# Optimization experiments

Hardware: AMD Instinct MI355X
Metric: run time of the kernel (lower is better)

The kernel has to match this reference:

```python
import jax, jax.numpy as jnp
import numpy as np

N = 100000   # nodes
E = 1600000  # edges
G = 256      # graphs in batch
C_IN = 128
D = 64
EPS = 1e-5
SLOPE = 0.01  # torch LeakyReLU default


def gcn_conv(h_x, src, dst, w_edge, W, b):
    """GCNConv: linear -> symmetric-normalized scatter aggregation (+ self loops) -> bias."""
    n = h_x.shape[0]
    h = h_x @ W                                   # [N, D]
    # add self loops with weight 1
    loop = jnp.arange(n, dtype=src.dtype)
    s = jnp.concatenate([src, loop])
    d = jnp.concatenate([dst, loop])
    w = jnp.concatenate([w_edge, jnp.ones((n,), h_x.dtype)])
    deg = jax.ops.segment_sum(w, d, num_segments=n)  # degree on target nodes
    dinv = jnp.where(deg > 0, jax.lax.rsqrt(jnp.maximum(deg, 1e-12)), 0.0)
    norm = dinv[s] * w * dinv[d]                  # [E+N]
    msg = h[s] * norm[:, None]                    # gather + scale
    out = jax.ops.segment_sum(msg, d, num_segments=n)
    return out + b


def batch_norm(h, gamma, beta):
    mean = jnp.mean(h, axis=0)
    var = jnp.mean((h - mean) ** 2, axis=0)       # biased var (training-mode BN)
    return (h - mean) * jax.lax.rsqrt(var + EPS) * gamma + beta


def setup_inputs() -> dict:
    key = jax.random.key(0)
    ks = jax.random.split(key, 16)
    inp = {
        "x": jax.random.normal(ks[0], (N, C_IN), jnp.float32),
        "edge_index": jax.random.randint(ks[1], (2, E), 0, N, jnp.int32),
        "batch": jnp.sort(jax.random.randint(ks[2], (N,), 0, G, jnp.int32)),
        "edge_attr": jax.random.uniform(ks[3], (E,), jnp.float32),
        "W0": jax.random.normal(ks[4], (C_IN, D), jnp.float32) * 0.05,
        "b0": jnp.zeros((D,), jnp.float32),
        "g0": jnp.ones((D,), jnp.float32),
        "be0": jnp.zeros((D,), jnp.float32),
        "W1": jax.random.normal(ks[5], (D, D), jnp.float32) * 0.05,
        "b1": jnp.zeros((D,), jnp.float32),
        "g1": jnp.ones((D,), jnp.float32),
        "be1": jnp.zeros((D,), jnp.float32),
        "W2": jax.random.normal(ks[6], (D, D), jnp.float32) * 0.05,
        "b2": jnp.zeros((D,), jnp.float32),
        "W3": jax.random.normal(ks[7], (D, D), jnp.float32) * 0.05,
        "b3": jnp.zeros((D,), jnp.float32),
        "Wfc": jax.random.normal(ks[8], (2 * D, 1), jnp.float32) * 0.05,
        "bfc": jnp.zeros((1,), jnp.float32),
    }
    return inp


def reference(x, edge_index, batch, edge_attr,
              W0, b0, g0, be0, W1, b1, g1, be1, W2, b2, W3, b3, Wfc, bfc):
    src, dst = edge_index[0], edge_index[1]
    lrelu = lambda h: jax.nn.leaky_relu(h, SLOPE)

    h = lrelu(batch_norm(gcn_conv(x, src, dst, edge_attr, W0, b0), g0, be0))
    h = lrelu(batch_norm(gcn_conv(h, src, dst, edge_attr, W1, b1), g1, be1))
    h = lrelu(gcn_conv(h, src, dst, edge_attr, W2, b2))  # dropout is identity in eval
    h = lrelu(gcn_conv(h, src, dst, edge_attr, W3, b3))

    mx = jax.ops.segment_max(h, batch, num_segments=G)
    sm = jax.ops.segment_sum(h, batch, num_segments=G)
    cnt = jax.ops.segment_sum(jnp.ones((N,), h.dtype), batch, num_segments=G)
    mean = sm / jnp.maximum(cnt, 1.0)[:, None]
    pooled = jnp.concatenate([mx, mean], axis=1)   # [G, 2D]
    return pooled @ Wfc + bfc                      # [G, 1]
```

## Files before the change

### kernel.cpp

```cpp
#include <hip/hip_runtime.h>
#include <math.h>

#define LRELU_SLOPE 0.01f
#define BN_EPS 1e-5f
#define WQ_SCALE 1048576.0f
#define WQ_INV   9.5367431640625e-7f

static inline int ceil_div(int a, int b) { return (a + b - 1) / b; }

__device__ __forceinline__ unsigned short f2bf(float f) {
  unsigned int u = __float_as_uint(f);
  u = u + 0x7FFFu + ((u >> 16) & 1u);
  return (unsigned short)(u >> 16);
}
#define BF2F(u) __uint_as_float(((unsigned int)(u)) << 16)

__launch_bounds__(1024)
__global__ void b1_hist(const int* __restrict__ ei, int* __restrict__ histT,
                        int E, int chunk, int nbuck) {
  __shared__ unsigned int hist[1024];
  const int t = threadIdx.x;
  const int blk = blockIdx.x;
  hist[t] = 0;
  __syncthreads();
  const int e0 = blk * chunk;
  const int e1 = min(e0 + chunk, E);
  for (int e = e0 + t; e < e1; e += 1024) {
    int d = ei[E + e];
    atomicAdd(&hist[d >> 7], 1u);
  }
  __syncthreads();
  if (t < nbuck) histT[(size_t)t * 256 + blk] = (int)hist[t];
}

__global__ void scan1i(const int* __restrict__ in, int* __restrict__ out,
                       int* __restrict__ bsum, int n) {
  __shared__ int lds[256];
  const int t = threadIdx.x;
  const int base = blockIdx.x * 1024 + t * 4;
  int v0 = 0, v1 = 0, v2 = 0, v3 = 0;
  if (base + 0 < n) v0 = in[base + 0];
  if (base + 1 < n) v1 = in[base + 1];
  if (base + 2 < n) v2 = in[base + 2];
  if (base + 3 < n) v3 = in[base + 3];
  int s = v0 + v1 + v2 + v3;
  lds[t] = s;
  __syncthreads();
#pragma unroll
  for (int off = 1; off < 256; off <<= 1) {
    int y = 0;
    if (t >= off) y = lds[t - off];
    __syncthreads();
    if (t >= off) lds[t] += y;
    __syncthreads();
  }
  int incl = lds[t];
  int excl = incl - s;
  if (base + 0 < n) out[base + 0] = excl;
  if (base + 1 < n) out[base + 1] = excl + v0;
  if (base + 2 < n) out[base + 2] = excl + v0 + v1;
  if (base + 3 < n) out[base + 3] = excl + v0 + v1 + v2;
  if (t == 255) bsum[blockIdx.x] = incl;
}

__global__ void scan2i(int* __restrict__ bsum, int nb) {
  __shared__ int lds[256];
  int t = threadIdx.x;
  int v = (t < nb) ? bsum[t] : 0;
  lds[t] = v;
  __syncthreads();
#pragma unroll
  for (int off = 1; off < 256; off <<= 1) {
    int y = 0;
    if (t >= off) y = lds[t - off];
    __syncthreads();
    if (t >= off) lds[t] += y;
    __syncthreads();
  }
  if (t < nb) bsum[t] = lds[t] - v;
}

__global__ void scan3i(int* __restrict__ data, const int* __restrict__ bscan, int n) {
  int i = blockIdx.x * blockDim.x + threadIdx.x;
  if (i < n) data[i] += bscan[i >> 10];
}

__launch_bounds__(1024)
__global__ void b3_scatter(const int* __restrict__ ei, const float* __restrict__ w,
                           const int* __restrict__ histS,
                           unsigned long long* __restrict__ bucketed,
                           int E, int chunk, int nbuck) {
  __shared__ unsigned int cursor[1024];
  const int t = threadIdx.x;
  const int blk = blockIdx.x;
  cursor[t] = (t < nbuck) ? (unsigned int)histS[(size_t)t * 256 + blk] : 0u;
  __syncthreads();
  const int e0 = blk * chunk;
  const int e1 = min(e0 + chunk, E);
  for (int e = e0 + t; e < e1; e += 1024) {
    int s = ei[e];
    int d = ei[E + e];
    unsigned int pos = atomicAdd(&cursor[d >> 7], 1u);
    unsigned long long p = ((unsigned long long)(unsigned int)(d & 127) << 57) |
                           ((unsigned long long)(unsigned int)s << 32) |
                           (unsigned long long)__float_as_uint(w[e]);
    bucketed[pos] = p;
  }
}

__launch_bounds__(256)
__global__ void c1_degree(const unsigned long long* __restrict__ bucketed,
                          const int* __restrict__ histS,
                          int* __restrict__ rowstart, float* __restrict__ dinv,
                          int N, int E, int nbuck) {
  __shared__ unsigned int cnt[128], wsum[128];
  __shared__ int sc[128];
  const int t = threadIdx.x;
  const int b = blockIdx.x;
  if (t < 128) { cnt[t] = 0; wsum[t] = 0; }
  __syncthreads();
  const int r0 = histS[(size_t)b * 256];
  const int r1 = (b + 1 < nbuck) ? histS[(size_t)(b + 1) * 256] : E;
  for (int r = r0 + t; r < r1; r += 256) {
    unsigned long long p = bucketed[r];
    int d7 = (int)(p >> 57);
    float wv = __uint_as_float((unsigned int)p);
    atomicAdd(&cnt[d7], 1u);
    atomicAdd(&wsum[d7], (unsigned int)__float2uint_rn(wv * WQ_SCALE));
  }
  __syncthreads();
  if (t < 128) sc[t] = (int)cnt[t];
  __syncthreads();
#pragma unroll
  for (int off = 1; off < 128; off <<= 1) {
    int y = 0;
    if (t < 128 && t >= off) y = sc[t - off];
    __syncthreads();
    if (t < 128 && t >= off) sc[t] += y;
    __syncthreads();
  }
  if (t < 128) {
    int node = (b << 7) + t;
    if (node < N) {
      rowstart[node] = r0 + sc[t] - (int)cnt[t];
      float deg = 1.0f + (float)wsum[t] * WQ_INV;
      dinv[node] = rsqrtf(deg);
    }
  }
  if (b == 0 && t == 0) rowstart[N] = E;
}

__launch_bounds__(256)
__global__ void c2_fill(const unsigned long long* __restrict__ bucketed,
                        const int* __restrict__ histS,
                        const int* __restrict__ rowstart, const float* __restrict__ dinv,
                        unsigned long long* __restrict__ colval,
                        int N, int E, int nbuck) {
  __shared__ unsigned int cursor[128];
  const int t = threadIdx.x;
  const int b = blockIdx.x;
  if (t < 128) {
    int node = (b << 7) + t;
    cursor[t] = (node < N) ? (unsigned int)rowstart[node] : 0u;
  }
  __syncthreads();
  const int r0 = histS[(size_t)b * 256];
  const int r1 = (b + 1 < nbuck) ? histS[(size_t)(b + 1) * 256] : E;
  for (int r = r0 + t; r < r1; r += 256) {
    unsigned long long p = bucketed[r];
    int d7 = (int)(p >> 57);
    int s = (int)((p >> 32) & 0x1FFFFFF);
    float wv = __uint_as_float((unsigned int)p);
    unsigned int pos = atomicAdd(&cursor[d7], 1u);
    float v = wv * dinv[s];
    colval[pos] = ((unsigned long long)(unsigned int)s << 32) |
                  (unsigned long long)__float_as_uint(v);
  }
}

template <int K, int BN>
__launch_bounds__(256, 4)
__global__ void k_gemm(const float* __restrict__ X, const float* __restrict__ W,
                       unsigned short* __restrict__ H16,
                       const float* __restrict__ s, const float* __restrict__ ss,
                       const float* __restrict__ g, const float* __restrict__ be,
                       int N) {
  __shared__ float Xl[64 * 68];
  __shared__ float Wl[64 * 64];
  __shared__ float scaleC[64], shiftC[64];
  const int t = threadIdx.x;
  const int tx = t & 15;
  const int ty = t >> 4;
  const int n0 = blockIdx.x * 64;

  if (BN) {
    if (t < 64) {
      float invN = 1.0f / (float)N;
      float mean = s[t] * invN;
      float var = ss[t] * invN - mean * mean;
      float sc = g[t] * rsqrtf(var + BN_EPS);
      scaleC[t] = sc;
      shiftC[t] = be[t] - mean * sc;
    }
  }

  float4 acc[4];
#pragma unroll
  for (int r = 0; r < 4; ++r) acc[r] = make_float4(0.f, 0.f, 0.f, 0.f);

  for (int kt = 0; kt < K; kt += 64) {
    __syncthreads();
#pragma unroll
    for (int l = 0; l < 4; ++l) {
      int idx = t + l * 256;
      int node = idx >> 4;
      int kq = idx & 15;
      int gn = n0 + node;
      float4 v = make_float4(0.f, 0.f, 0.f, 0.f);
      if (gn < N) v = *(const float4*)(X + (size_t)gn * K + kt + 4 * kq);
      int kb = 4 * kq;
      if (BN) {
        float a;
        a = v.x * scaleC[kb + 0] + shiftC[kb + 0]; v.x = (a > 0.f) ? a : LRELU_SLOPE * a;
        a = v.y * scaleC[kb + 1] + shiftC[kb + 1]; v.y = (a > 0.f) ? a : LRELU_SLOPE * a;
        a = v.z * scaleC[kb + 2] + shiftC[kb + 2]; v.z = (a > 0.f) ? a : LRELU_SLOPE * a;
        a = v.w * scaleC[kb + 3] + shiftC[kb + 3]; v.w = (a > 0.f) ? a : LRELU_SLOPE * a;
      }
      Xl[(kb + 0) * 68 + node] = v.x;
      Xl[(kb + 1) * 68 + node] = v.y;
      Xl[(kb + 2) * 68 + node] = v.z;
      Xl[(kb + 3) * 68 + node] = v.w;
    }
#pragma unroll
    for (int l = 0; l < 4; ++l) {
      int idx = t + l * 256;
      ((float4*)Wl)[idx] = *(const float4*)(W + (size_t)(kt + (idx >> 4)) * 64 + 4 * (idx & 15));
    }
    __syncthreads();
#pragma unroll 8
    for (int k = 0; k < 64; ++k) {
      float4 xv = *(const float4*)(Xl + k * 68 + 4 * ty);
      float4 wv = *(const float4*)(Wl + k * 64 + 4 * tx);
      acc[0].x += xv.x * wv.x; acc[0].y += xv.x * wv.y; acc[0].z += xv.x * wv.z; acc[0].w += xv.x * wv.w;
      acc[1].x += xv.y * wv.x; acc[1].y += xv.y * wv.y; acc[1].z += xv.y * wv.z; acc[1].w += xv.y * wv.w;
      acc[2].x += xv.z * wv.x; acc[2].y += xv.z * wv.y; acc[2].z += xv.z * wv.z; acc[2].w += xv.z * wv.w;
      acc[3].x += xv.w * wv.x; acc[3].y += xv.w * wv.y; acc[3].z += xv.w * wv.z; acc[3].w += xv.w * wv.w;
    }
  }
#pragma unroll
  for (int r = 0; r < 4; ++r) {
    int gn = n0 + 4 * ty + r;
    if (gn < N) {
      ushort4 o;
      o.x = f2bf(acc[r].x); o.y = f2bf(acc[r].y);
      o.z = f2bf(acc[r].z); o.w = f2bf(acc[r].w);
      *(ushort4*)(H16 + (size_t)gn * 64 + 4 * tx) = o;
    }
  }
}

__launch_bounds__(256)
__global__ void k_agg(const unsigned short* __restrict__ h16, float* __restrict__ hout,
                      const float* __restrict__ bias, const float* __restrict__ dinv,
                      const int* __restrict__ rowstart,
                      const unsigned long long* __restrict__ colval,
                      int N, int apply_lrelu) {
  const int t = threadIdx.x;
  const int grp = t >> 4;
  const int lane = t & 15;
  const int d = blockIdx.x * 16 + grp;
  if (d >= N) return;
  const int r0 = rowstart[d];
  const int r1 = rowstart[d + 1];
  float4 a0 = make_float4(0.f, 0.f, 0.f, 0.f);
  float4 a1 = make_float4(0.f, 0.f, 0.f, 0.f);
  float4 a2 = make_float4(0.f, 0.f, 0.f, 0.f);
  float4 a3 = make_float4(0.f, 0.f, 0.f, 0.f);
  int r = r0;
  for (; r + 8 <= r1; r += 8) {
    unsigned long long cv0 = colval[r + 0];
    unsigned long long cv1 = colval[r + 1];
    unsigned long long cv2 = colval[r + 2];
    unsigned long long cv3 = colval[r + 3];
    unsigned long long cv4 = colval[r + 4];
    unsigned long long cv5 = colval[r + 5];
    unsigned long long cv6 = colval[r + 6];
    unsigned long long cv7 = colval[r + 7];
    ushort4 h0 = *(const ushort4*)(h16 + ((size_t)(cv0 >> 32)) * 64 + lane * 4);
    ushort4 h1 = *(const ushort4*)(h16 + ((size_t)(cv1 >> 32)) * 64 + lane * 4);
    ushort4 h2 = *(const ushort4*)(h16 + ((size_t)(cv2 >> 32)) * 64 + lane * 4);
    ushort4 h3 = *(const ushort4*)(h16 + ((size_t)(cv3 >> 32)) * 64 + lane * 4);
    ushort4 h4 = *(const ushort4*)(h16 + ((size_t)(cv4 >> 32)) * 64 + lane * 4);
    ushort4 h5 = *(const ushort4*)(h16 + ((size_t)(cv5 >> 32)) * 64 + lane * 4);
    ushort4 h6 = *(const ushort4*)(h16 + ((size_t)(cv6 >> 32)) * 64 + lane * 4);
    ushort4 h7 = *(const ushort4*)(h16 + ((size_t)(cv7 >> 32)) * 64 + lane * 4);
    float v0 = __uint_as_float((unsigned int)cv0);
    float v1 = __uint_as_float((unsigned int)cv1);
    float v2 = __uint_as_float((unsigned int)cv2);
    float v3 = __uint_as_float((unsigned int)cv3);
    float v4 = __uint_as_float((unsigned int)cv4);
    float v5 = __uint_as_float((unsigned int)cv5);
    float v6 = __uint_as_float((unsigned int)cv6);
    float v7 = __uint_as_float((unsigned int)cv7);
    a0.x += v0 * BF2F(h0.x); a0.y += v0 * BF2F(h0.y); a0.z += v0 * BF2F(h0.z); a0.w += v0 * BF2F(h0.w);
    a1.x += v1 * BF2F(h1.x); a1.y += v1 * BF2F(h1.y); a1.z += v1 * BF2F(h1.z); a1.w += v1 * BF2F(h1.w);
    a2.x += v2 * BF2F(h2.x); a2.y += v2 * BF2F(h2.y); a2.z += v2 * BF2F(h2.z); a2.w += v2 * BF2F(h2.w);
    a3.x += v3 * BF2F(h3.x); a3.y += v3 * BF2F(h3.y); a3.z += v3 * BF2F(h3.z); a3.w += v3 * BF2F(h3.w);
    a0.x += v4 * BF2F(h4.x); a0.y += v4 * BF2F(h4.y); a0.z += v4 * BF2F(h4.z); a0.w += v4 * BF2F(h4.w);
    a1.x += v5 * BF2F(h5.x); a1.y += v5 * BF2F(h5.y); a1.z += v5 * BF2F(h5.z); a1.w += v5 * BF2F(h5.w);
    a2.x += v6 * BF2F(h6.x); a2.y += v6 * BF2F(h6.y); a2.z += v6 * BF2F(h6.z); a2.w += v6 * BF2F(h6.w);
    a3.x += v7 * BF2F(h7.x); a3.y += v7 * BF2F(h7.y); a3.z += v7 * BF2F(h7.z); a3.w += v7 * BF2F(h7.w);
  }
  for (; r + 4 <= r1; r += 4) {
    unsigned long long cv0 = colval[r + 0];
    unsigned long long cv1 = colval[r + 1];
    unsigned long long cv2 = colval[r + 2];
    unsigned long long cv3 = colval[r + 3];
    ushort4 h0 = *(const ushort4*)(h16 + ((size_t)(cv0 >> 32)) * 64 + lane * 4);
    ushort4 h1 = *(const ushort4*)(h16 + ((size_t)(cv1 >> 32)) * 64 + lane * 4);
    ushort4 h2 = *(const ushort4*)(h16 + ((size_t)(cv2 >> 32)) * 64 + lane * 4);
    ushort4 h3 = *(const ushort4*)(h16 + ((size_t)(cv3 >> 32)) * 64 + lane * 4);
    float v0 = __uint_as_float((unsigned int)cv0);
    float v1 = __uint_as_float((unsigned int)cv1);
    float v2 = __uint_as_float((unsigned int)cv2);
    float v3 = __uint_as_float((unsigned int)cv3);
    a0.x += v0 * BF2F(h0.x); a0.y += v0 * BF2F(h0.y); a0.z += v0 * BF2F(h0.z); a0.w += v0 * BF2F(h0.w);
    a1.x += v1 * BF2F(h1.x); a1.y += v1 * BF2F(h1.y); a1.z += v1 * BF2F(h1.z); a1.w += v1 * BF2F(h1.w);
    a2.x += v2 * BF2F(h2.x); a2.y += v2 * BF2F(h2.y); a2.z += v2 * BF2F(h2.z); a2.w += v2 * BF2F(h2.w);
    a3.x += v3 * BF2F(h3.x); a3.y += v3 * BF2F(h3.y); a3.z += v3 * BF2F(h3.z); a3.w += v3 * BF2F(h3.w);
  }
  for (; r < r1; ++r) {
    unsigned long long cv = colval[r];
    float v = __uint_as_float((unsigned int)cv);
    ushort4 hv = *(const ushort4*)(h16 + ((size_t)(cv >> 32)) * 64 + lane * 4);
    a0.x += v * BF2F(hv.x); a0.y += v * BF2F(hv.y); a0.z += v * BF2F(hv.z); a0.w += v * BF2F(hv.w);
  }
  float4 acc;
  acc.x = (a0.x + a1.x) + (a2.x + a3.x);
  acc.y = (a0.y + a1.y) + (a2.y + a3.y);
  acc.z = (a0.z + a1.z) + (a2.z + a3.z);
  acc.w = (a0.w + a1.w) + (a2.w + a3.w);
  float di = dinv[d];
  float di2 = di * di;
  ushort4 hd4 = *(const ushort4*)(h16 + (size_t)d * 64 + lane * 4);
  float4 b4 = *(const float4*)(bias + lane * 4);
  float4 o;
  o.x = di * acc.x + di2 * BF2F(hd4.x) + b4.x;
  o.y = di * acc.y + di2 * BF2F(hd4.y) + b4.y;
  o.z = di * acc.z + di2 * BF2F(hd4.z) + b4.z;
  o.w = di * acc.w + di2 * BF2F(hd4.w) + b4.w;
  if (apply_lrelu) {
    o.x = (o.x > 0.f) ? o.x : LRELU_SLOPE * o.x;
    o.y = (o.y > 0.f) ? o.y : LRELU_SLOPE * o.y;
    o.z = (o.z > 0.f) ? o.z : LRELU_SLOPE * o.z;
    o.w = (o.w > 0.f) ? o.w : LRELU_SLOPE * o.w;
  }
  *(float4*)(hout + (size_t)d * 64 + lane * 4) = o;
}

__launch_bounds__(256)
__global__ void k_stats(const float* __restrict__ h, float* __restrict__ partial, int N) {
  __shared__ float ls[256], lss[256];
  const int t = threadIdx.x;
  const int c = t & 63;
  float a = 0.f, a2 = 0.f;
  for (int n = blockIdx.x * 4 + (t >> 6); n < N; n += gridDim.x * 4) {
    float v = h[(size_t)n * 64 + c];
    a += v;
    a2 += v * v;
  }
  ls[t] = a;
  lss[t] = a2;
  __syncthreads();
  if (t < 64) {
    a = ls[t] + ls[t + 64] + ls[t + 128] + ls[t + 192];
    a2 = lss[t] + lss[t + 64] + lss[t + 128] + lss[t + 192];
    partial[blockIdx.x * 128 + t] = a;
    partial[blockIdx.x * 128 + 64 + t] = a2;
  }
}

__global__ void k_stats_reduce(const float* __restrict__ partial, float* __restrict__ s,
                               float* __restrict__ ss, int nb) {
  __shared__ float red[256];
  const int c = blockIdx.x;
  const int t = threadIdx.x;
  float a = 0.f;
  for (int b = t; b < nb; b += 256) a += partial[(size_t)b * 128 + c];
  red[t] = a;
  __syncthreads();
  for (int st = 128; st >= 1; st >>= 1) {
    if (t < st) red[t] += red[t + st];
    __syncthreads();
  }
  if (t == 0) {
    if (c < 64) s[c] = red[0];
    else ss[c - 64] = red[0];
  }
}

__global__ void k_gbounds(const int* __restrict__ batch, int* __restrict__ gstart,
                          int N, int G) {
  int i = blockIdx.x * blockDim.x + threadIdx.x;
  if (i >= N) return;
  int b = batch[i];
  int prev = (i == 0) ? -1 : batch[i - 1];
  for (int g = prev + 1; g <= b; ++g) gstart[g] = i;
  if (i == N - 1) {
    for (int g = b + 1; g <= G; ++g) gstart[g] = N;
  }
}

__launch_bounds__(256)
__global__ void k_pool(const float* __restrict__ h, const int* __restrict__ gstart,
                       const float* __restrict__ Wfc, const float* __restrict__ bfc,
                       float* __restrict__ out, int G) {
  __shared__ float lmx[256], lsm[256], red[128];
  const int g = blockIdx.x;
  const int t = threadIdx.x;
  const int c = t & 63;
  const int sub = t >> 6;
  const int n0 = gstart[g];
  const int n1 = gstart[g + 1];
  float mx = -INFINITY, sm = 0.f;
  for (int n = n0 + sub; n < n1; n += 4) {
    float v = h[(size_t)n * 64 + c];
    mx = fmaxf(mx, v);
    sm += v;
  }
  lmx[t] = mx;
  lsm[t] = sm;
  __syncthreads();
  if (t < 64) {
    mx = fmaxf(fmaxf(lmx[t], lmx[t + 64]), fmaxf(lmx[t + 128], lmx[t + 192]));
    sm = lsm[t] + lsm[t + 64] + lsm[t + 128] + lsm[t + 192];
    float cntf = (float)(n1 - n0);
    float mean = sm / fmaxf(cntf, 1.0f);
    red[t] = mx * Wfc[t];
    red[t + 64] = mean * Wfc[64 + t];
  }
  __syncthreads();
  for (int st = 64; st >= 1; st >>= 1) {
    if (t < st) red[t] += red[t + st];
    __syncthreads();
  }
  if (t == 0) out[g] = red[0] + bfc[0];
}

extern "C" void kernel_launch(void* const* d_in, const int* in_sizes, int n_in,
                              void* d_out, int out_size, void* d_ws, size_t ws_size,
                              hipStream_t stream) {
  const float* x = (const float*)d_in[0];
  const int* ei = (const int*)d_in[1];
  const int* batch = (const int*)d_in[2];
  const float* eattr = (const float*)d_in[3];
  const float* W0 = (const float*)d_in[4];
  const float* b0 = (const float*)d_in[5];
  const float* g0 = (const float*)d_in[6];
  const float* be0 = (const float*)d_in[7];
  const float* W1 = (const float*)d_in[8];
  const float* b1 = (const float*)d_in[9];
  const float* g1 = (const float*)d_in[10];
  const float* be1 = (const float*)d_in[11];
  const float* W2 = (const float*)d_in[12];
  const float* b2 = (const float*)d_in[13];
  const float* W3 = (const float*)d_in[14];
  const float* b3 = (const float*)d_in[15];
  const float* Wfc = (const float*)d_in[16];
  const float* bfc = (const float*)d_in[17];
  float* out = (float*)d_out;

  const int N = in_sizes[2];
  const int E = in_sizes[3];
  const int CIN = in_sizes[0] / N;
  const int G = out_size;
  const int nbuck = ceil_div(N, 128);
  const int chunk = ceil_div(E, 256);
  const int M = nbuck * 256;

  size_t off = 0;
  auto alloc = [&](size_t bytes) -> void* {
    void* p = (char*)d_ws + off;
    off += (bytes + 255) & ~(size_t)255;
    return p;
  };
  int* histT = (int*)alloc((size_t)1024 * 256 * 4);
  int* histS = (int*)alloc((size_t)1024 * 256 * 4);
  int* bsum = (int*)alloc(1024 * 4);
  unsigned long long* bucketed = (unsigned long long*)alloc((size_t)E * 8);
  float* dinv = (float*)alloc((size_t)N * 4);
  int* rowstart = (int*)alloc((size_t)(N + 1) * 4);
  unsigned long long* colval = (unsigned long long*)alloc((size_t)E * 8);
  float* A = (float*)alloc((size_t)N * 64 * 4);
  float* B = (float*)alloc((size_t)N * 64 * 4);
  unsigned short* H16 = (unsigned short*)alloc((size_t)N * 64 * 2);
  float* sums = (float*)alloc(256 * 4);
  float* partial = (float*)alloc(256 * 128 * 4);
  int* gstart = (int*)alloc((size_t)(G + 1) * 4);
  (void)ws_size; (void)n_in; (void)CIN;

  b1_hist<<<256, 1024, 0, stream>>>(ei, histT, E, chunk, nbuck);
  const int nbs = ceil_div(M, 1024);
  scan1i<<<nbs, 256, 0, stream>>>(histT, histS, bsum, M);
  scan2i<<<1, 256, 0, stream>>>(bsum, nbs);
  scan3i<<<ceil_div(M, 256), 256, 0, stream>>>(histS, bsum, M);
  b3_scatter<<<256, 1024, 0, stream>>>(ei, eattr, histS, bucketed, E, chunk, nbuck);
  c1_degree<<<nbuck, 256, 0, stream>>>(bucketed, histS, rowstart, dinv, N, E, nbuck);
  c2_fill<<<nbuck, 256, 0, stream>>>(bucketed, histS, rowstart, dinv, colval, N, E, nbuck);
  k_gbounds<<<ceil_div(N, 256), 256, 0, stream>>>(batch, gstart, N, G);

  k_gemm<128, 0><<<ceil_div(N, 64), 256, 0, stream>>>(x, W0, H16, nullptr, nullptr, nullptr, nullptr, N);
  k_agg<<<ceil_div(N, 16), 256, 0, stream>>>(H16, B, b0, dinv, rowstart, colval, N, 0);
  k_stats<<<256, 256, 0, stream>>>(B, partial, N);
  k_stats_reduce<<<128, 256, 0, stream>>>(partial, sums + 0, sums + 64, 256);

  k_gemm<64, 1><<<ceil_div(N, 64), 256, 0, stream>>>(B, W1, H16, sums + 0, sums + 64, g0, be0, N);
  k_agg<<<ceil_div(N, 16), 256, 0, stream>>>(H16, A, b1, dinv, rowstart, colval, N, 0);
  k_stats<<<256, 256, 0, stream>>>(A, partial, N);
  k_stats_reduce<<<128, 256, 0, stream>>>(partial, sums + 128, sums + 192, 256);

  k_gemm<64, 1><<<ceil_div(N, 64), 256, 0, stream>>>(A, W2, H16, sums + 128, sums + 192, g1, be1, N);
  k_agg<<<ceil_div(N, 16), 256, 0, stream>>>(H16, B, b2, dinv, rowstart, colval, N, 1);

  k_gemm<64, 0><<<ceil_div(N, 64), 256, 0, stream>>>(B, W3, H16, nullptr, nullptr, nullptr, nullptr, N);
  k_agg<<<ceil_div(N, 16), 256, 0, stream>>>(H16, A, b3, dinv, rowstart, colval, N, 1);

  k_pool<<<G, 256, 0, stream>>>(A, gstart, Wfc, bfc, out, G);
}
```

Before: 490.3 us.

## Use fp16 MFMA for node GEMMs and fuse BN statistics into aggregation

The dense per-layer GEMM now converts inputs and weights to fp16 in LDS and uses 16x16x32 MFMA instructions in place of scalar FMA tiles. BatchNorm sum and sum-of-squares partials are computed inside the aggregation kernel via a block reduction, which removes the separate stats kernel and its re-read of the N×64 activations. The cost is fp16 rounding of the GEMM inputs and a much larger partial buffer (one row per aggregation block) for the stats reduce. The output store is now scattered 2-byte writes.

```diff
diff --git a/kernel.cpp b/kernel.cpp
--- a/kernel.cpp
+++ b/kernel.cpp
@@ -7,6 +7,11 @@
 #define WQ_INV   9.5367431640625e-7f
 
 static inline int ceil_div(int a, int b) { return (a + b - 1) / b; }
+
+typedef _Float16 f16;
+typedef f16 h4_t __attribute__((ext_vector_type(4)));
+typedef f16 h8_t __attribute__((ext_vector_type(8)));
+typedef float f32x4 __attribute__((ext_vector_type(4)));
 
 __device__ __forceinline__ unsigned short f2bf(float f) {
   unsigned int u = __float_as_uint(f);
@@ -185,12 +190,12 @@
                        const float* __restrict__ s, const float* __restrict__ ss,
                        const float* __restrict__ g, const float* __restrict__ be,
                        int N) {
-  __shared__ float Xl[64 * 68];
-  __shared__ float Wl[64 * 64];
+  constexpr int KP = K + 8;
+  constexpr int KQ = K / 4;
+  __shared__ f16 Xl[64 * KP];
+  __shared__ f16 Wt[64 * KP];
   __shared__ float scaleC[64], shiftC[64];
   const int t = threadIdx.x;
-  const int tx = t & 15;
-  const int ty = t >> 4;
   const int n0 = blockIdx.x * 64;
 
   if (BN) {
@@ -202,76 +207,91 @@
       scaleC[t] = sc;
       shiftC[t] = be[t] - mean * sc;
     }
-  }
-
-  float4 acc[4];
+    __syncthreads();
+  }
+
+  for (int idx = t; idx < 64 * KQ; idx += 256) {
+    int row = idx / KQ;
+    int kq = idx % KQ;
+    int gn = n0 + row;
+    float4 v = make_float4(0.f, 0.f, 0.f, 0.f);
+    if (gn < N) v = *(const float4*)(X + (size_t)gn * K + 4 * kq);
+    if (BN) {
+      int c = 4 * kq;
+      float a;
+      a = v.x * scaleC[c + 0] + shiftC[c + 0]; v.x = (a > 0.f) ? a : LRELU_SLOPE * a;
+      a = v.y * scaleC[c + 1] + shiftC[c + 1]; v.y = (a > 0.f) ? a : LRELU_SLOPE * a;
+      a = v.z * scaleC[c + 2] + shiftC[c + 2]; v.z = (a > 0.f) ? a : LRELU_SLOPE * a;
+      a = v.w * scaleC[c + 3] + shiftC[c + 3]; v.w = (a > 0.f) ? a : LRELU_SLOPE * a;
+    }
+    h4_t hv = { (f16)v.x, (f16)v.y, (f16)v.z, (f16)v.w };
+    *(h4_t*)(Xl + row * KP + 4 * kq) = hv;
+  }
+  for (int idx = t; idx < K * 16; idx += 256) {
+    int k = idx >> 4;
+    int c4 = idx & 15;
+    float4 wv = *(const float4*)(W + (size_t)k * 64 + 4 * c4);
+    Wt[(4 * c4 + 0) * KP + k] = (f16)wv.x;
+    Wt[(4 * c4 + 1) * KP + k] = (f16)wv.y;
+    Wt[(4 * c4 + 2) * KP + k] = (f16)wv.z;
+    Wt[(4 * c4 + 3) * KP + k] = (f16)wv.w;
+  }
+  __syncthreads();
+
+  const int lane = t & 63;
+  const int wv = t >> 6;
+  const int fr = lane & 15;
+  const int fc = lane >> 4;
+
+  f32x4 acc0 = {0.f, 0.f, 0.f, 0.f};
+  f32x4 acc1 = {0.f, 0.f, 0.f, 0.f};
+  f32x4 acc2 = {0.f, 0.f, 0.f, 0.f};
+  f32x4 acc3 = {0.f, 0.f, 0.f, 0.f};
+
+  const f16* ap = Xl + (16 * wv + fr) * KP + 8 * fc;
+  const f16* bp0 = Wt + (0 + fr) * KP + 8 * fc;
+  const f16* bp1 = Wt + (16 + fr) * KP + 8 * fc;
+  const f16* bp2 = Wt + (32 + fr) * KP + 8 * fc;
+  const f16* bp3 = Wt + (48 + fr) * KP + 8 * fc;
+
 #pragma unroll
-  for (int r = 0; r < 4; ++r) acc[r] = make_float4(0.f, 0.f, 0.f, 0.f);
-
-  for (int kt = 0; kt < K; kt += 64) {
-    __syncthreads();
-#pragma unroll
-    for (int l = 0; l < 4; ++l) {
-      int idx = t + l * 256;
-      int node = idx >> 4;
-      int kq = idx & 15;
-      int gn = n0 + node;
-      float4 v = make_float4(0.f, 0.f, 0.f, 0.f);
-      if (gn < N) v = *(const float4*)(X + (size_t)gn * K + kt + 4 * kq);
-      int kb = 4 * kq;
-      if (BN) {
-        float a;
-        a = v.x * scaleC[kb + 0] + shiftC[kb + 0]; v.x = (a > 0.f) ? a : LRELU_SLOPE * a;
-        a = v.y * scaleC[kb + 1] + shiftC[kb + 1]; v.y = (a > 0.f) ? a : LRELU_SLOPE * a;
-        a = v.z * scaleC[kb + 2] + shiftC[kb + 2]; v.z = (a > 0.f) ? a : LRELU_SLOPE * a;
-        a = v.w * scaleC[kb + 3] + shiftC[kb + 3]; v.w = (a > 0.f) ? a : LRELU_SLOPE * a;
-      }
-      Xl[(kb + 0) * 68 + node] = v.x;
-      Xl[(kb + 1) * 68 + node] = v.y;
-      Xl[(kb + 2) * 68 + node] = v.z;
-      Xl[(kb + 3) * 68 + node] = v.w;
-    }
-#pragma unroll
-    for (int l = 0; l < 4; ++l) {
-      int idx = t + l * 256;
-      ((float4*)Wl)[idx] = *(const float4*)(W + (size_t)(kt + (idx >> 4)) * 64 + 4 * (idx & 15));
-    }
-    __syncthreads();
-#pragma unroll 8
-    for (int k = 0; k < 64; ++k) {
-      float4 xv = *(const float4*)(Xl + k * 68 + 4 * ty);
-      float4 wv = *(const float4*)(Wl + k * 64 + 4 * tx);
-      acc[0].x += xv.x * wv.x; acc[0].y += xv.x * wv.y; acc[0].z += xv.x * wv.z; acc[0].w += xv.x * wv.w;
-      acc[1].x += xv.y * wv.x; acc[1].y += xv.y * wv.y; acc[1].z += xv.y * wv.z; acc[1].w += xv.y * wv.w;
-      acc[2].x += xv.z * wv.x; acc[2].y += xv.z * wv.y; acc[2].z += xv.z * wv.z; acc[2].w += xv.z * wv.w;
-      acc[3].x += xv.w * wv.x; acc[3].y += xv.w * wv.y; acc[3].z += xv.w * wv.z; acc[3].w += xv.w * wv.w;
-    }
-  }
+  for (int kt = 0; kt < K; kt += 32) {
+    h8_t a = *(const h8_t*)(ap + kt);
+    acc0 = __builtin_amdgcn_mfma_f32_16x16x32_f16(a, *(const h8_t*)(bp0 + kt), acc0, 0, 0, 0);
+    acc1 = __builtin_amdgcn_mfma_f32_16x16x32_f16(a, *(const h8_t*)(bp1 + kt), acc1, 0, 0, 0);
+    acc2 = __builtin_amdgcn_mfma_f32_16x16x32_f16(a, *(const h8_t*)(bp2 + kt), acc2, 0, 0, 0);
+    acc3 = __builtin_amdgcn_mfma_f32_16x16x32_f16(a, *(const h8_t*)(bp3 + kt), acc3, 0, 0, 0);
+  }
+
 #pragma unroll
   for (int r = 0; r < 4; ++r) {
-    int gn = n0 + 4 * ty + r;
-    if (gn < N) {
-      ushort4 o;
-      o.x = f2bf(acc[r].x); o.y = f2bf(acc[r].y);
-      o.z = f2bf(acc[r].z); o.w = f2bf(acc[r].w);
-      *(ushort4*)(H16 + (size_t)gn * 64 + 4 * tx) = o;
+    int node = n0 + 16 * wv + 4 * fc + r;
+    if (node < N) {
+      size_t base = (size_t)node * 64 + fr;
+      H16[base + 0]  = f2bf(acc0[r]);
+      H16[base + 16] = f2bf(acc1[r]);
+      H16[base + 32] = f2bf(acc2[r]);
+      H16[base + 48] = f2bf(acc3[r]);
     }
   }
 }
 
+template <int STATS, int LRELU>
 __launch_bounds__(256)
 __global__ void k_agg(const unsigned short* __restrict__ h16, float* __restrict__ hout,
                       const float* __restrict__ bias, const float* __restrict__ dinv,
                       const int* __restrict__ rowstart,
                       const unsigned long long* __restrict__ colval,
-                      int N, int apply_lrelu) {
+                      float* __restrict__ partial, int N) {
+  __shared__ float4 rs[STATS ? 256 : 1];
+  __shared__ float4 rq[STATS ? 256 : 1];
   const int t = threadIdx.x;
   const int grp = t >> 4;
   const int lane = t & 15;
   const int d = blockIdx.x * 16 + grp;
-  if (d >= N) return;
-  const int r0 = rowstart[d];
-  const int r1 = rowstart[d + 1];
+  const bool valid = (d < N);
+  int r0 = 0, r1 = 0;
+  if (valid) { r0 = rowstart[d]; r1 = rowstart[d + 1]; }
   float4 a0 = make_float4(0.f, 0.f, 0.f, 0.f);
   float4 a1 = make_float4(0.f, 0.f, 0.f, 0.f);
   float4 a2 = make_float4(0.f, 0.f, 0.f, 0.f);
@@ -340,43 +360,45 @@
   acc.y = (a0.y + a1.y) + (a2.y + a3.y);
   acc.z = (a0.z + a1.z) + (a2.z + a3.z);
   acc.w = (a0.w + a1.w) + (a2.w + a3.w);
-  float di = dinv[d];
+  float di = valid ? dinv[d] : 0.f;
   float di2 = di * di;
-  ushort4 hd4 = *(const ushort4*)(h16 + (size_t)d * 64 + lane * 4);
+  ushort4 hd4 = make_ushort4(0, 0, 0, 0);
+  if (valid) hd4 = *(const ushort4*)(h16 + (size_t)d * 64 + lane * 4);
   float4 b4 = *(const float4*)(bias + lane * 4);
   float4 o;
   o.x = di * acc.x + di2 * BF2F(hd4.x) + b4.x;
   o.y = di * acc.y + di2 * BF2F(hd4.y) + b4.y;
   o.z = di * acc.z + di2 * BF2F(hd4.z) + b4.z;
   o.w = di * acc.w + di2 * BF2F(hd4.w) + b4.w;
-  if (apply_lrelu) {
+  if (LRELU) {
     o.x = (o.x > 0.f) ? o.x : LRELU_SLOPE * o.x;
     o.y = (o.y > 0.f) ? o.y : LRELU_SLOPE * o.y;
     o.z = (o.z > 0.f) ? o.z : LRELU_SLOPE * o.z;
     o.w = (o.w > 0.f) ? o.w : LRELU_SLOPE * o.w;
   }
-  *(float4*)(hout + (size_t)d * 64 + lane * 4) = o;
-}
-
-__launch_bounds__(256)
-__global__ void k_stats(const float* __restrict__ h, float* __restrict__ partial, int N) {
-  __shared__ float ls[256], lss[256];
-  const int t = threadIdx.x;
-  const int c = t & 63;
-  float a = 0.f, a2 = 0.f;
-  for (int n = blockIdx.x * 4 + (t >> 6); n < N; n += gridDim.x * 4) {
-    float v = h[(size_t)n * 64 + c];
-    a += v;
-    a2 += v * v;
-  }
-  ls[t] = a;
-  lss[t] = a2;
-  __syncthreads();
-  if (t < 64) {
-    a = ls[t] + ls[t + 64] + ls[t + 128] + ls[t + 192];
-    a2 = lss[t] + lss[t + 64] + lss[t + 128] + lss[t + 192];
-    partial[blockIdx.x * 128 + t] = a;
-    partial[blockIdx.x * 128 + 64 + t] = a2;
+  if (!valid) o = make_float4(0.f, 0.f, 0.f, 0.f);
+  if (valid) *(float4*)(hout + (size_t)d * 64 + lane * 4) = o;
+
+  if (STATS) {
+    rs[t] = o;
+    rq[t] = make_float4(o.x * o.x, o.y * o.y, o.z * o.z, o.w * o.w);
+    __syncthreads();
+#pragma unroll
+    for (int st = 8; st >= 1; st >>= 1) {
+      if ((t >> 4) < st) {
+        float4 sa = rs[t], sb = rs[t + st * 16];
+        float4 qa = rq[t], qb = rq[t + st * 16];
+        rs[t] = make_float4(sa.x + sb.x, sa.y + sb.y, sa.z + sb.z, sa.w + sb.w);
+        rq[t] = make_float4(qa.x + qb.x, qa.y + qb.y, qa.z + qb.z, qa.w + qb.w);
+      }
+      __syncthreads();
+    }
+    if (t < 16) {
+      float4 sv = rs[t], qv = rq[t];
+      float* ps = partial + (size_t)blockIdx.x * 128 + 4 * t;
+      ps[0] = sv.x; ps[1] = sv.y; ps[2] = sv.z; ps[3] = sv.w;
+      ps[64] = qv.x; ps[65] = qv.y; ps[66] = qv.z; ps[67] = qv.w;
+    }
   }
 }
 
@@ -477,6 +499,7 @@
   const int nbuck = ceil_div(N, 128);
   const int chunk = ceil_div(E, 256);
   const int M = nbuck * 256;
+  const int nag = ceil_div(N, 16);
 
   size_t off = 0;
   auto alloc = [&](size_t bytes) -> void* {
@@ -495,7 +518,7 @@
   float* B = (float*)alloc((size_t)N * 64 * 4);
   unsigned short* H16 = (unsigned short*)alloc((size_t)N * 64 * 2);
   float* sums = (float*)alloc(256 * 4);
-  float* partial = (float*)alloc(256 * 128 * 4);
+  float* partial = (float*)alloc((size_t)nag * 128 * 4);
   int* gstart = (int*)alloc((size_t)(G + 1) * 4);
   (void)ws_size; (void)n_in; (void)CIN;
 
@@ -510,20 +533,18 @@
   k_gbounds<<<ceil_div(N, 256), 256, 0, stream>>>(batch, gstart, N, G);
 
   k_gemm<128, 0><<<ceil_div(N, 64), 256, 0, stream>>>(x, W0, H16, nullptr, nullptr, nullptr, nullptr, N);
-  k_agg<<<ceil_div(N, 16), 256, 0, stream>>>(H16, B, b0, dinv, rowstart, colval, N, 0);
-  k_stats<<<256, 256, 0, stream>>>(B, partial, N);
-  k_stats_reduce<<<128, 256, 0, stream>>>(partial, sums + 0, sums + 64, 256);
+  k_agg<1, 0><<<nag, 256, 0, stream>>>(H16, B, b0, dinv, rowstart, colval, partial, N);
+  k_stats_reduce<<<128, 256, 0, stream>>>(partial, sums + 0, sums + 64, nag);
 
   k_gemm<64, 1><<<ceil_div(N, 64), 256, 0, stream>>>(B, W1, H16, sums + 0, sums + 64, g0, be0, N);
-  k_agg<<<ceil_div(N, 16), 256, 0, stream>>>(H16, A, b1, dinv, rowstart, colval, N, 0);
-  k_stats<<<256, 256, 0, stream>>>(A, partial, N);
-  k_stats_reduce<<<128, 256, 0, stream>>>(partial, sums + 128, sums + 192, 256);
+  k_agg<1, 0><<<nag, 256, 0, stream>>>(H16, A, b1, dinv, rowstart, colval, partial, N);
+  k_stats_reduce<<<128, 256, 0, stream>>>(partial, sums + 128, sums + 192, nag);
 
   k_gemm<64, 1><<<ceil_div(N, 64), 256, 0, stream>>>(A, W2, H16, sums + 128, sums + 192, g1, be1, N);
-  k_agg<<<ceil_div(N, 16), 256, 0, stream>>>(H16, B, b2, dinv, rowstart, colval, N, 1);
+  k_agg<0, 1><<<nag, 256, 0, stream>>>(H16, B, b2, dinv, rowstart, colval, nullptr, N);
 
   k_gemm<64, 0><<<ceil_div(N, 64), 256, 0, stream>>>(B, W3, H16, nullptr, nullptr, nullptr, nullptr, N);
-  k_agg<<<ceil_div(N, 16), 256, 0, stream>>>(H16, A, b3, dinv, rowstart, colval, N, 1);
+  k_agg<0, 1><<<nag, 256, 0, stream>>>(H16, A, b3, dinv, rowstart, colval, nullptr, N);
 
   k_pool<<<G, 256, 0, stream>>>(A, gstart, Wfc, bfc, out, G);
 }
```

Measured after the change: 436.3 us. 11.0% less time.
